# Performance work log

Measured on AMD Instinct MI355X. Metric: run time of the kernel, lower is better.

The kernel has to match this reference:

```python
import jax, jax.numpy as jnp
import numpy as np

B, S, D, H, P, K = 2, 1025, 1024, 16, 1024, 32
HD = D // H
G = int(np.sqrt(P))
TEMP = 0.1
CANTOR_W = 0.3
SCALE = HD ** -0.5
EPS_LN = 1e-5


def _layernorm(x, w, b):
    m = jnp.mean(x, axis=-1, keepdims=True)
    v = jnp.mean((x - m) ** 2, axis=-1, keepdims=True)
    return (x - m) * jax.lax.rsqrt(v + EPS_LN) * w + b


def _l2norm(x):
    n = jnp.sqrt(jnp.sum(x * x, axis=-1, keepdims=True))
    return x / jnp.maximum(n, 1e-12)


def _cantor_bias():
    idx = np.arange(P)
    xg, yg = idx % G, idx // G
    s = xg + yg
    z = (s * (s + 1) // 2 + yg).astype(np.float32)
    fp = z / max(z.max(), 1.0)
    dist = np.abs(fp[None, :] - fp[:, None])
    aff = 1.0 - dist
    np.fill_diagonal(aff, -1e9)
    return jnp.asarray(aff * CANTOR_W, dtype=jnp.float32)


def setup_inputs() -> dict:
    key = jax.random.key(0)
    ks = jax.random.split(key, 16)
    std = 0.02
    def w(k, *shape):
        return jax.random.normal(k, shape, dtype=jnp.float32) * std
    inp = {
        'x': jax.random.normal(ks[0], (B, S, D), dtype=jnp.float32),
        'norm1_w': jnp.ones((D,), jnp.float32), 'norm1_b': jnp.zeros((D,), jnp.float32),
        'rq_w': w(ks[1], D, D), 'rq_b': jnp.zeros((D,), jnp.float32),
        'rk_w': w(ks[2], D, D), 'rk_b': jnp.zeros((D,), jnp.float32),
        'pos_bias': _cantor_bias(),
        'qkv_w': w(ks[3], 3 * D, D), 'qkv_b': jnp.zeros((3 * D,), jnp.float32),
        'proj_w': w(ks[4], D, D), 'proj_b': jnp.zeros((D,), jnp.float32),
        'norm2_w': jnp.ones((D,), jnp.float32), 'norm2_b': jnp.zeros((D,), jnp.float32),
        'fc1_w': w(ks[5], 4 * D, D), 'fc1_b': jnp.zeros((4 * D,), jnp.float32),
        'fc2_w': w(ks[6], D, 4 * D), 'fc2_b': jnp.zeros((D,), jnp.float32),
    }
    return inp


def reference(x, norm1_w, norm1_b, rq_w, rq_b, rk_w, rk_b, pos_bias,
              qkv_w, qkv_b, proj_w, proj_b, norm2_w, norm2_b,
              fc1_w, fc1_b, fc2_w, fc2_b):
    x_norm = _layernorm(x, norm1_w, norm1_b)
    # ---- router: content-based top-k wormhole routes over patches ----
    xp = x_norm[:, 1:, :]                                   # [B,P,D]
    q_r = _l2norm(xp @ rq_w.T + rq_b)
    k_r = _l2norm(xp @ rk_w.T + rk_b)
    scores = jnp.einsum('bpd,bqd->bpq', q_r, k_r) + pos_bias[None]
    eye = jnp.eye(P, dtype=bool)
    scores = jnp.where(eye[None], -1e9, scores)
    topk_scores, routes = jax.lax.top_k(scores / TEMP, K)   # [B,P,K]
    route_w = jax.nn.softmax(topk_scores, axis=-1)          # [B,P,K]
    # ---- qkv ----
    qkv = (x_norm @ qkv_w.T + qkv_b).reshape(B, S, 3, H, HD)
    qkv = jnp.transpose(qkv, (2, 0, 3, 1, 4))               # [3,B,H,S,hd]
    Q, Kf, V = qkv[0], qkv[1], qkv[2]
    # CLS token: dense attention over all positions
    Qc = Q[:, :, :1, :]
    attn_cls = jax.nn.softmax(jnp.einsum('bhqd,bhkd->bhqk', Qc, Kf) * SCALE, axis=-1)
    out_cls = jnp.einsum('bhqk,bhkd->bhqd', attn_cls, V)    # [B,H,1,hd]
    # Patches: sparse gather attention via wormhole routes
    Qp, Kp, Vp = Q[:, :, 1:], Kf[:, :, 1:], V[:, :, 1:]     # [B,H,P,hd]
    gather = jax.vmap(lambda t, r: t[:, r])                 # t:[H,P,hd], r:[P,K] -> [H,P,K,hd]
    Kg = gather(Kp, routes)                                  # [B,H,P,K,hd]
    Vg = gather(Vp, routes)
    sp = jnp.einsum('bhpd,bhpkd->bhpk', Qp, Kg) * SCALE
    sp = sp + jnp.clip(jnp.log(route_w), -10.0, None)[:, None]
    attn_p = jax.nn.softmax(sp, axis=-1)
    out_p = jnp.einsum('bhpk,bhpkd->bhpd', attn_p, Vg)      # [B,H,P,hd]
    out = jnp.concatenate([out_cls, out_p], axis=2)          # [B,H,S,hd]
    out = jnp.transpose(out, (0, 2, 1, 3)).reshape(B, S, D)
    x = x + (out @ proj_w.T + proj_b)
    h = _layernorm(x, norm2_w, norm2_b)
    h = jax.nn.gelu(h @ fc1_w.T + fc1_b, approximate=False)
    x = x + (h @ fc2_w.T + fc2_b)
    return x
```

## Files before the change

### kernel.cpp

```cpp
#include <hip/hip_runtime.h>
#include <hip/hip_bf16.h>
#include <math.h>

typedef unsigned short u16;
typedef __attribute__((ext_vector_type(8))) short short8;
typedef __attribute__((ext_vector_type(4))) float f32x4;

#define B_ 2
#define S_ 1025
#define D_ 1024
#define H_ 16
#define HD_ 64
#define P_ 1024
#define K_ 32
#define NS_ 16

static constexpr float TEMP_ = 0.1f;
static constexpr float SCALE_ = 0.125f;
static constexpr float EPS_LN_ = 1e-5f;

__device__ __forceinline__ float bf2f(u16 u) {
  unsigned int t = ((unsigned int)u) << 16;
  float f;
  __builtin_memcpy(&f, &t, 4);
  return f;
}
__device__ __forceinline__ u16 f2bf(float f) {
  __hip_bfloat16 h = __float2bfloat16(f);
  u16 u;
  __builtin_memcpy(&u, &h, 2);
  return u;
}
__device__ __forceinline__ float gelu_f(float x) {
  return 0.5f * x * (1.0f + erff(x * 0.70710678118654752f));
}

typedef __attribute__((address_space(1))) const unsigned int gas_u32;
typedef __attribute__((address_space(3))) unsigned int las_u32;
__device__ __forceinline__ void g2l16(const void* g, void* l) {
  __builtin_amdgcn_global_load_lds((gas_u32*)g, (las_u32*)l, 16, 0, 0);
}

__global__ __launch_bounds__(256) void conv4_kernel(
    const float* __restrict__ s0, int n0, const float* __restrict__ s1, int n1,
    const float* __restrict__ s2, int n2, const float* __restrict__ s3, int n3,
    u16* __restrict__ dst) {
  const int e = (blockIdx.x * 256 + threadIdx.x) * 4;
  const float* src;
  int off;
  if (e < n0) { src = s0; off = e; }
  else if (e < n0 + n1) { src = s1; off = e - n0; }
  else if (e < n0 + n1 + n2) { src = s2; off = e - n0 - n1; }
  else if (e < n0 + n1 + n2 + n3) { src = s3; off = e - n0 - n1 - n2; }
  else return;
  float4 t = *reinterpret_cast<const float4*>(src + off);
  ushort4 o;
  o.x = f2bf(t.x); o.y = f2bf(t.y); o.z = f2bf(t.z); o.w = f2bf(t.w);
  *reinterpret_cast<ushort4*>(dst + e) = o;
}

__global__ __launch_bounds__(256) void init_addb(const float* __restrict__ a,
                                                 const float* __restrict__ bias,
                                                 float* __restrict__ out) {
  const long long base = (long long)blockIdx.x * D_;
#pragma unroll
  for (int u = 0; u < 4; ++u) {
    int d = threadIdx.x + u * 256;
    out[base + d] = a[base + d] + bias[d];
  }
}

__global__ __launch_bounds__(256) void init_scores(const float* __restrict__ pos,
                                                   float* __restrict__ scores) {
  const int bp = blockIdx.x;
  const int p = bp & (P_ - 1);
  const long long base = (long long)bp * P_;
#pragma unroll
  for (int u = 0; u < 4; ++u) {
    int q = threadIdx.x + u * 256;
    float v = pos[(long long)p * P_ + q];
    if (p == q) v = -1e9f;
    scores[base + q] = v;
  }
}

__device__ __forceinline__ float block_sum256(float v, float* red4) {
  for (int off = 32; off > 0; off >>= 1) v += __shfl_down(v, off);
  if ((threadIdx.x & 63) == 0) red4[threadIdx.x >> 6] = v;
  __syncthreads();
  float r = red4[0] + red4[1] + red4[2] + red4[3];
  __syncthreads();
  return r;
}
__device__ __forceinline__ float block_max256(float v, float* red4) {
  for (int off = 32; off > 0; off >>= 1) v = fmaxf(v, __shfl_down(v, off));
  if ((threadIdx.x & 63) == 0) red4[threadIdx.x >> 6] = v;
  __syncthreads();
  float r = fmaxf(fmaxf(red4[0], red4[1]), fmaxf(red4[2], red4[3]));
  __syncthreads();
  return r;
}

__global__ __launch_bounds__(256) void ln_kernel(const float* __restrict__ x,
                                                 const float* __restrict__ w,
                                                 const float* __restrict__ b,
                                                 u16* __restrict__ out) {
  __shared__ float red4[4];
  const long long base = (long long)blockIdx.x * D_;
  float v[4];
  float s = 0.f, ss = 0.f;
#pragma unroll
  for (int u = 0; u < 4; ++u) {
    int d = threadIdx.x + u * 256;
    float f = x[base + d];
    v[u] = f; s += f; ss += f * f;
  }
  float tot = block_sum256(s, red4);
  float tot2 = block_sum256(ss, red4);
  float mean = tot * (1.0f / D_);
  float var = tot2 * (1.0f / D_) - mean * mean;
  float rstd = rsqrtf(var + EPS_LN_);
#pragma unroll
  for (int u = 0; u < 4; ++u) {
    int d = threadIdx.x + u * 256;
    out[base + d] = f2bf((v[u] - mean) * rstd * w[d] + b[d]);
  }
}

__global__ __launch_bounds__(256) void l2norm2_kernel(u16* __restrict__ qr,
                                                      u16* __restrict__ kr) {
  __shared__ float red4[4];
  const int row = blockIdx.x;
  u16* x = (row < 2048) ? qr + (long long)row * D_
                        : kr + (long long)(row - 2048) * D_;
  float v[4];
  float ss = 0.f;
#pragma unroll
  for (int u = 0; u < 4; ++u) {
    int d = threadIdx.x + u * 256;
    v[u] = bf2f(x[d]);
    ss += v[u] * v[u];
  }
  float tot = block_sum256(ss, red4);
  float inv = 1.0f / fmaxf(sqrtf(tot), 1e-12f);
#pragma unroll
  for (int u = 0; u < 4; ++u) {
    int d = threadIdx.x + u * 256;
    x[d] = f2bf(v[u] * inv);
  }
}

template <int MODE>
__device__ __forceinline__ void gemm_body(
    u16* sA, u16* sW,
    const u16* __restrict__ A, long long a_off, const u16* __restrict__ W,
    int N, int M, int Kd, int klen, int rpb, long long a_bs, long long w_bs,
    const float* __restrict__ bias, const float* __restrict__ bias2, int bias_off,
    u16* __restrict__ outU, u16* __restrict__ outU2, float* __restrict__ outF,
    int bx, int by, int bz) {
  const int tid = threadIdx.x;
  const int lane = tid & 63;
  const int q4 = lane >> 4;
  const int r16 = lane & 15;
  const int wave = tid >> 6;
  const int wr = (wave & 1) * 32;
  const int wc = (wave >> 1) * 64;
  const int row0 = by * 64;
  const int col0 = bx * 128;
  const int batch = row0 / rpb;
  const u16* Ab = A + a_off + (long long)batch * a_bs +
                  (long long)(row0 - batch * rpb) * Kd;
  const u16* Wb = W + (long long)batch * w_bs + (long long)col0 * Kd;
  const int rmax = N - 1 - row0;
  const int srow = tid >> 3;
  const int kx = ((tid & 7) ^ (srow & 7)) * 8;
  const int kbeg = bz * klen;
  const int niter = klen >> 6;
  f32x4 acc[2][4] = {};
  for (int it = 0; it < niter; ++it) {
    const int k0 = kbeg + it * 64;
#pragma unroll
    for (int c = 0; c < 2; ++c) {
      const int rg = c * 32 + srow;
      g2l16(Ab + (long long)min(rg, rmax) * Kd + kx + k0, &sA[c * 2048 + tid * 8]);
    }
#pragma unroll
    for (int c = 0; c < 4; ++c) {
      const int rg = c * 32 + srow;
      g2l16(Wb + (long long)rg * Kd + kx + k0, &sW[c * 2048 + tid * 8]);
    }
    __builtin_amdgcn_s_waitcnt(0);
    __syncthreads();
#pragma unroll
    for (int s = 0; s < 2; ++s) {
      short8 a[2], b[4];
      const int ks = ((s * 4 + q4) ^ (r16 & 7)) * 8;
#pragma unroll
      for (int i = 0; i < 2; ++i)
        a[i] = *reinterpret_cast<const short8*>(&sA[(wr + i * 16 + r16) * 64 + ks]);
#pragma unroll
      for (int j = 0; j < 4; ++j)
        b[j] = *reinterpret_cast<const short8*>(&sW[(wc + j * 16 + r16) * 64 + ks]);
#pragma unroll
      for (int i = 0; i < 2; ++i)
#pragma unroll
        for (int j = 0; j < 4; ++j)
          acc[i][j] = __builtin_amdgcn_mfma_f32_16x16x32_bf16(a[i], b[j],
                                                              acc[i][j], 0, 0, 0);
    }
    __syncthreads();
  }
#pragma unroll
  for (int i = 0; i < 2; ++i) {
#pragma unroll
    for (int reg = 0; reg < 4; ++reg) {
      const int n = row0 + wr + i * 16 + q4 * 4 + reg;
      if (n >= N) continue;
      const long long nrow = (long long)n * M;
#pragma unroll
      for (int j = 0; j < 4; ++j) {
        const int m = col0 + wc + j * 16 + r16;
        float v = acc[i][j][reg];
        if (MODE == 0) {
          if (m < 1024) outU[(long long)n * 1024 + m] = f2bf(v + bias[m]);
          else outU2[(long long)n * 1024 + m - 1024] = f2bf(v + bias2[m - 1024]);
        } else if (MODE == 2) {
          outU[nrow + m] = f2bf(v + bias[bias_off + m]);
        } else if (MODE == 3) {
          outU[nrow + m] = f2bf(gelu_f(v + bias[bias_off + m]));
        } else {
          unsafeAtomicAdd(&outF[nrow + m], v);
        }
      }
    }
  }
}

__device__ __forceinline__ int xcd_swz(int orig, int nwg) {
  return (orig & 7) * (nwg >> 3) + (orig >> 3);
}

template <int MODE>
__global__ __launch_bounds__(256, 6) void mfma_gemm(
    const u16* __restrict__ A, long long a_off, const u16* __restrict__ W,
    int N, int M, int Kd, int klen, int rpb, long long a_bs, long long w_bs,
    const float* __restrict__ bias, const float* __restrict__ bias2, int bias_off,
    u16* __restrict__ outU, u16* __restrict__ outU2, float* __restrict__ outF) {
  __shared__ u16 sA[64 * 64];
  __shared__ u16 sW[128 * 64];
  const int gx = gridDim.x, gy = gridDim.y;
  const int nwg = gx * gy * gridDim.z;
  const int orig = blockIdx.x + gx * (blockIdx.y + gy * blockIdx.z);
  const int swz = xcd_swz(orig, nwg);
  const int bx = swz % gx;
  const int t = swz / gx;
  const int by = t % gy;
  const int bz = t / gy;
  gemm_body<MODE>(sA, sW, A, a_off, W, N, M, Kd, klen, rpb, a_bs, w_bs,
                  bias, bias2, bias_off, outU, outU2, outF, bx, by, bz);
}

__global__ __launch_bounds__(256, 6) void fused_rqk_qkv(
    const u16* __restrict__ xnorm, const u16* __restrict__ wslot,
    const float* __restrict__ rq_b, const float* __restrict__ rk_b,
    const float* __restrict__ qkv_b,
    u16* __restrict__ qr, u16* __restrict__ kr, u16* __restrict__ qkvb) {
  __shared__ u16 sA[64 * 64];
  __shared__ u16 sW[128 * 64];
  const int id = xcd_swz(blockIdx.x, 1304);
  if (id < 512) {
    gemm_body<0>(sA, sW, xnorm, 1024LL, wslot,
                 2048, 2048, 1024, 1024, 1024, (long long)S_ * D_, 0LL,
                 rq_b, rk_b, 0, qr, kr, nullptr, id & 15, id >> 4, 0);
  } else {
    const int id2 = id - 512;
    gemm_body<2>(sA, sW, xnorm, 0LL, wslot + (2 << 20),
                 2050, 3072, 1024, 1024, 2050, 0LL, 0LL,
                 qkv_b, nullptr, 0, qkvb, nullptr, nullptr, id2 % 24, id2 / 24, 0);
  }
}

__global__ __launch_bounds__(256) void topk_kernel(const float* __restrict__ scores,
                                                   int* __restrict__ routes,
                                                   float* __restrict__ logw) {
  const int row = blockIdx.x * 4 + (threadIdx.x >> 6);
  const int lane = threadIdx.x & 63;
  const float* sr = scores + (long long)row * P_;
  float v[16];
#pragma unroll
  for (int j = 0; j < 16; ++j) v[j] = sr[j * 64 + lane];
  float selv = 0.f;
  int seli = 0;
  for (int t = 0; t < K_; ++t) {
    float bv = v[0];
    int bj = 0;
#pragma unroll
    for (int j = 1; j < 16; ++j)
      if (v[j] > bv) { bv = v[j]; bj = j; }
    int bi = bj * 64 + lane;
#pragma unroll
    for (int off = 1; off < 64; off <<= 1) {
      float ov = __shfl_xor(bv, off);
      int oi = __shfl_xor(bi, off);
      if (ov > bv || (ov == bv && oi < bi)) { bv = ov; bi = oi; }
    }
    if (lane == t) { selv = bv; seli = bi; }
    if ((bi & 63) == lane) v[bi >> 6] = -3.0e38f;
  }
  const float sc = selv * (1.0f / TEMP_);
  const float mt = __shfl(sc, 0);
  float e = (lane < K_) ? expf(sc - mt) : 0.f;
  float sum = e;
#pragma unroll
  for (int off = 1; off < 64; off <<= 1) sum += __shfl_xor(sum, off);
  if (lane < K_) {
    const float lw = sc - mt - logf(sum);
    logw[(long long)row * K_ + lane] = fmaxf(lw, -10.0f);
    routes[(long long)row * K_ + lane] = seli;
  }
}

__global__ __launch_bounds__(256) void attn_cls_p1(const u16* __restrict__ qkv,
                                                   float* __restrict__ part) {
  __shared__ float qs[HD_];
  __shared__ float lg[65];
  __shared__ float red4[4];
  __shared__ float sacc[4][HD_];
  const int ck = blockIdx.x;
  const int bh = blockIdx.y;
  const int b = bh >> 4, h = bh & 15;
  const int tid = threadIdx.x;
  const int lane = tid & 63;
  const int wv = tid >> 6;
  const int s0 = ck * 65;
  const int rows = min(65, S_ - s0);
  const long long base = (long long)b * S_ * 3072;
  if (tid < HD_) qs[tid] = bf2f(qkv[base + h * HD_ + tid]);
  __syncthreads();
  float lmax = -3.0e38f;
  if (tid < rows) {
    const u16* kp = qkv + base + (long long)(s0 + tid) * 3072 + 1024 + h * HD_;
    float d = 0.f;
#pragma unroll
    for (int c = 0; c < 8; ++c) {
      short8 kv = *reinterpret_cast<const short8*>(kp + c * 8);
#pragma unroll
      for (int e = 0; e < 8; ++e) d += qs[c * 8 + e] * bf2f((u16)kv[e]);
    }
    d *= SCALE_;
    lg[tid] = d;
    lmax = d;
  }
  const float m = block_max256(lmax, red4);
  float e = 0.f;
  if (tid < rows) {
    e = expf(lg[tid] - m);
    lg[tid] = e;
  }
  const float l = block_sum256(e, red4);
  __syncthreads();
  float acc = 0.f;
  for (int r = wv; r < rows; r += 4)
    acc += lg[r] * bf2f(qkv[base + (long long)(s0 + r) * 3072 + 2048 + h * HD_ + lane]);
  sacc[wv][lane] = acc;
  __syncthreads();
  float* pc = part + ((long long)bh * NS_ + ck) * 66;
  if (tid < HD_)
    pc[tid] = sacc[0][tid] + sacc[1][tid] + sacc[2][tid] + sacc[3][tid];
  if (tid == 64) pc[64] = m;
  if (tid == 65) pc[65] = l;
}

__global__ __launch_bounds__(64) void attn_cls_p2(const float* __restrict__ part,
                                                  u16* __restrict__ out) {
  const int bh = blockIdx.x;
  const int b = bh >> 4, h = bh & 15;
  const int tid = threadIdx.x;
  const float* pb = part + (long long)bh * NS_ * 66;
  float M = -3.0e38f;
#pragma unroll
  for (int c = 0; c < NS_; ++c) M = fmaxf(M, pb[c * 66 + 64]);
  float L = 0.f, a = 0.f;
#pragma unroll
  for (int c = 0; c < NS_; ++c) {
    const float w = expf(pb[c * 66 + 64] - M);
    L += pb[c * 66 + 65] * w;
    a += pb[c * 66 + tid] * w;
  }
  out[(long long)b * S_ * D_ + h * HD_ + tid] = f2bf(a / L);
}

__global__ __launch_bounds__(64) void attn_patch_kernel(const u16* __restrict__ qkv,
                                                        const int* __restrict__ routes,
                                                        const float* __restrict__ logw,
                                                        u16* __restrict__ out) {
  __shared__ float qs[HD_];
  __shared__ float wk[K_];
  __shared__ int sidx[K_];
  const int bid = blockIdx.x;
  const int h = bid & 15;
  const int p = (bid >> 4) & (P_ - 1);
  const int b = bid >> 14;
  const int tid = threadIdx.x;
  const long long base = (long long)b * S_ * 3072;
  qs[tid] = bf2f(qkv[base + (long long)(1 + p) * 3072 + h * HD_ + tid]);
  __syncthreads();
  float lg = -3.0e38f;
  if (tid < K_) {
    const long long ro = ((long long)(b * P_ + p)) * K_ + tid;
    const int r = routes[ro];
    sidx[tid] = r;
    const u16* kp = qkv + base + (long long)(1 + r) * 3072 + 1024 + h * HD_;
    float d = 0.f;
#pragma unroll
    for (int c = 0; c < 8; ++c) {
      short8 kv = *reinterpret_cast<const short8*>(kp + c * 8);
#pragma unroll
      for (int e = 0; e < 8; ++e) d += qs[c * 8 + e] * bf2f((u16)kv[e]);
    }
    lg = d * SCALE_ + logw[ro];
  }
  float m = lg;
#pragma unroll
  for (int off = 1; off < 32; off <<= 1) m = fmaxf(m, __shfl_xor(m, off));
  float e = (tid < K_) ? expf(lg - m) : 0.f;
  float sum = e;
#pragma unroll
  for (int off = 1; off < 32; off <<= 1) sum += __shfl_xor(sum, off);
  if (tid < K_) wk[tid] = e / sum;
  __syncthreads();
  float acc = 0.f;
#pragma unroll 4
  for (int k = 0; k < K_; ++k)
    acc += wk[k] * bf2f(qkv[base + (long long)(1 + sidx[k]) * 3072 + 2048 + h * HD_ + tid]);
  out[((long long)b * S_ + 1 + p) * D_ + h * HD_ + tid] = f2bf(acc);
}

extern "C" void kernel_launch(void* const* d_in, const int* in_sizes, int n_in,
                              void* d_out, int out_size, void* d_ws, size_t ws_size,
                              hipStream_t stream) {
  const float* x      = (const float*)d_in[0];
  const float* n1w    = (const float*)d_in[1];
  const float* n1b    = (const float*)d_in[2];
  const float* rq_w   = (const float*)d_in[3];
  const float* rq_b   = (const float*)d_in[4];
  const float* rk_w   = (const float*)d_in[5];
  const float* rk_b   = (const float*)d_in[6];
  const float* pos    = (const float*)d_in[7];
  const float* qkv_w  = (const float*)d_in[8];
  const float* qkv_b  = (const float*)d_in[9];
  const float* proj_w = (const float*)d_in[10];
  const float* proj_b = (const float*)d_in[11];
  const float* n2w    = (const float*)d_in[12];
  const float* n2b    = (const float*)d_in[13];
  const float* fc1_w  = (const float*)d_in[14];
  const float* fc1_b  = (const float*)d_in[15];
  const float* fc2_w  = (const float*)d_in[16];
  const float* fc2_b  = (const float*)d_in[17];
  float* out = (float*)d_out;

  char* mem = (char*)d_ws;
  int*   routes = (int*)mem;
  float* logw   = (float*)(mem + 262144);
  float* part   = (float*)(mem + 524288);
  u16*   wslot  = (u16*)(mem + 786432);
  u16*   xnorm  = (u16*)(mem + 17563648);
  u16*   qr     = (u16*)(mem + 21762048);
  u16*   attn   = qr;
  u16*   qkvb   = (u16*)(mem + 25960448);
  u16*   kr     = (u16*)(mem + 38555648);
  u16*   hbuf   = qkvb;
  float* scores = (float*)(mem + 42758144);
  float* x1     = (float*)(mem + 42758144);

  ln_kernel<<<B_ * S_, 256, 0, stream>>>(x, n1w, n1b, xnorm);

  conv4_kernel<<<6144, 256, 0, stream>>>(rq_w, 1 << 20, rk_w, 1 << 20,
                                         qkv_w, 3 << 20, proj_w, 1 << 20, wslot);

  fused_rqk_qkv<<<1304, 256, 0, stream>>>(xnorm, wslot, rq_b, rk_b, qkv_b,
                                          qr, kr, qkvb);

  l2norm2_kernel<<<4096, 256, 0, stream>>>(qr, kr);

  init_scores<<<B_ * P_, 256, 0, stream>>>(pos, scores);
  mfma_gemm<5><<<dim3(8, 32, 2), 256, 0, stream>>>(qr, 0LL, kr,
      2048, 1024, 1024, 512, 1024, 1LL << 20, 1LL << 20,
      nullptr, nullptr, 0, nullptr, nullptr, scores);

  topk_kernel<<<512, 256, 0, stream>>>(scores, routes, logw);

  attn_cls_p1<<<dim3(NS_, B_ * H_), 256, 0, stream>>>(qkvb, part);
  attn_cls_p2<<<B_ * H_, 64, 0, stream>>>(part, attn);
  attn_patch_kernel<<<B_ * P_ * H_, 64, 0, stream>>>(qkvb, routes, logw, attn);

  init_addb<<<B_ * S_, 256, 0, stream>>>(x, proj_b, x1);
  mfma_gemm<5><<<dim3(8, 33, 2), 256, 0, stream>>>(attn, 0LL, wslot + (5 << 20),
      2050, 1024, 1024, 512, 2050, 0LL, 0LL,
      nullptr, nullptr, 0, nullptr, nullptr, x1);

  conv4_kernel<<<8192, 256, 0, stream>>>(fc1_w, 1 << 22, fc2_w, 1 << 22,
                                         nullptr, 0, nullptr, 0, wslot);

  ln_kernel<<<B_ * S_, 256, 0, stream>>>(x1, n2w, n2b, xnorm);

  mfma_gemm<3><<<dim3(32, 33), 256, 0, stream>>>(xnorm, 0LL, wslot,
      2050, 4096, 1024, 1024, 2050, 0LL, 0LL,
      fc1_b, nullptr, 0, hbuf, nullptr, nullptr);
  init_addb<<<B_ * S_, 256, 0, stream>>>(x1, fc2_b, out);
  mfma_gemm<5><<<dim3(8, 33, 4), 256, 0, stream>>>(hbuf, 0LL, wslot + (1 << 22),
      2050, 1024, 4096, 1024, 2050, 0LL, 0LL,
      nullptr, nullptr, 0, nullptr, nullptr, out);
}
```

Before: 404.1 us.

## Replace split-K atomics with partial buffers reduced in consumer kernels

```diff
diff --git a/kernel.cpp b/kernel.cpp
--- a/kernel.cpp
+++ b/kernel.cpp
@@ -59,31 +59,6 @@
   *reinterpret_cast<ushort4*>(dst + e) = o;
 }
 
-__global__ __launch_bounds__(256) void init_addb(const float* __restrict__ a,
-                                                 const float* __restrict__ bias,
-                                                 float* __restrict__ out) {
-  const long long base = (long long)blockIdx.x * D_;
-#pragma unroll
-  for (int u = 0; u < 4; ++u) {
-    int d = threadIdx.x + u * 256;
-    out[base + d] = a[base + d] + bias[d];
-  }
-}
-
-__global__ __launch_bounds__(256) void init_scores(const float* __restrict__ pos,
-                                                   float* __restrict__ scores) {
-  const int bp = blockIdx.x;
-  const int p = bp & (P_ - 1);
-  const long long base = (long long)bp * P_;
-#pragma unroll
-  for (int u = 0; u < 4; ++u) {
-    int q = threadIdx.x + u * 256;
-    float v = pos[(long long)p * P_ + q];
-    if (p == q) v = -1e9f;
-    scores[base + q] = v;
-  }
-}
-
 __device__ __forceinline__ float block_sum256(float v, float* red4) {
   for (int off = 32; off > 0; off >>= 1) v += __shfl_down(v, off);
   if ((threadIdx.x & 63) == 0) red4[threadIdx.x >> 6] = v;
@@ -124,6 +99,46 @@
   for (int u = 0; u < 4; ++u) {
     int d = threadIdx.x + u * 256;
     out[base + d] = f2bf((v[u] - mean) * rstd * w[d] + b[d]);
+  }
+}
+
+__global__ __launch_bounds__(256) void ln2res_kernel(
+    const float* __restrict__ x, const float* __restrict__ pb,
+    const float* __restrict__ p0, const float* __restrict__ p1,
+    const float* __restrict__ w, const float* __restrict__ b,
+    float* __restrict__ x1, u16* __restrict__ out) {
+  __shared__ float red4[4];
+  const long long base = (long long)blockIdx.x * D_;
+  float v[4];
+  float s = 0.f, ss = 0.f;
+#pragma unroll
+  for (int u = 0; u < 4; ++u) {
+    int d = threadIdx.x + u * 256;
+    float f = x[base + d] + pb[d] + p0[base + d] + p1[base + d];
+    x1[base + d] = f;
+    v[u] = f; s += f; ss += f * f;
+  }
+  float tot = block_sum256(s, red4);
+  float tot2 = block_sum256(ss, red4);
+  float mean = tot * (1.0f / D_);
+  float var = tot2 * (1.0f / D_) - mean * mean;
+  float rstd = rsqrtf(var + EPS_LN_);
+#pragma unroll
+  for (int u = 0; u < 4; ++u) {
+    int d = threadIdx.x + u * 256;
+    out[base + d] = f2bf((v[u] - mean) * rstd * w[d] + b[d]);
+  }
+}
+
+__global__ __launch_bounds__(256) void fc2red_kernel(
+    const float* __restrict__ x1, const float* __restrict__ b,
+    const float* __restrict__ p0, const float* __restrict__ p1,
+    float* __restrict__ out) {
+  const long long base = (long long)blockIdx.x * D_;
+#pragma unroll
+  for (int u = 0; u < 4; ++u) {
+    int d = threadIdx.x + u * 256;
+    out[base + d] = x1[base + d] + b[d] + p0[base + d] + p1[base + d];
   }
 }
 
@@ -210,6 +225,7 @@
     }
     __syncthreads();
   }
+  const long long sbase = (MODE == 6) ? (long long)bz * bias_off : 0;
 #pragma unroll
   for (int i = 0; i < 2; ++i) {
 #pragma unroll
@@ -229,7 +245,7 @@
         } else if (MODE == 3) {
           outU[nrow + m] = f2bf(gelu_f(v + bias[bias_off + m]));
         } else {
-          unsafeAtomicAdd(&outF[nrow + m], v);
+          outF[sbase + nrow + m] = v;
         }
       }
     }
@@ -280,15 +296,24 @@
   }
 }
 
-__global__ __launch_bounds__(256) void topk_kernel(const float* __restrict__ scores,
+__global__ __launch_bounds__(256) void topk_kernel(const float* __restrict__ s0,
+                                                   const float* __restrict__ s1,
+                                                   const float* __restrict__ pos,
                                                    int* __restrict__ routes,
                                                    float* __restrict__ logw) {
   const int row = blockIdx.x * 4 + (threadIdx.x >> 6);
   const int lane = threadIdx.x & 63;
-  const float* sr = scores + (long long)row * P_;
+  const int p = row & (P_ - 1);
+  const float* r0 = s0 + (long long)row * P_;
+  const float* r1 = s1 + (long long)row * P_;
+  const float* pr = pos + (long long)p * P_;
   float v[16];
 #pragma unroll
-  for (int j = 0; j < 16; ++j) v[j] = sr[j * 64 + lane];
+  for (int j = 0; j < 16; ++j) {
+    const int q = j * 64 + lane;
+    float t = r0[q] + r1[q] + pr[q];
+    v[j] = (q == p) ? -1e9f : t;
+  }
   float selv = 0.f;
   int seli = 0;
   for (int t = 0; t < K_; ++t) {
@@ -470,8 +495,13 @@
   u16*   qkvb   = (u16*)(mem + 25960448);
   u16*   kr     = (u16*)(mem + 38555648);
   u16*   hbuf   = qkvb;
-  float* scores = (float*)(mem + 42758144);
   float* x1     = (float*)(mem + 42758144);
+  float* sc_p0 = (float*)(mem + 786432);
+  float* sc_p1 = (float*)(mem + 42758144);
+  float* pr_p0 = (float*)(mem + 25960448);
+  float* pr_p1 = (float*)(mem + 34357248);
+  float* fc_p0 = (float*)(mem + 0);
+  float* fc_p1 = (float*)(mem + 17563648);
 
   ln_kernel<<<B_ * S_, 256, 0, stream>>>(x, n1w, n1b, xnorm);
 
@@ -483,32 +513,31 @@
 
   l2norm2_kernel<<<4096, 256, 0, stream>>>(qr, kr);
 
-  init_scores<<<B_ * P_, 256, 0, stream>>>(pos, scores);
-  mfma_gemm<5><<<dim3(8, 32, 2), 256, 0, stream>>>(qr, 0LL, kr,
+  mfma_gemm<6><<<dim3(8, 32, 2), 256, 0, stream>>>(qr, 0LL, kr,
       2048, 1024, 1024, 512, 1024, 1LL << 20, 1LL << 20,
-      nullptr, nullptr, 0, nullptr, nullptr, scores);
-
-  topk_kernel<<<512, 256, 0, stream>>>(scores, routes, logw);
+      nullptr, nullptr, 10492928, nullptr, nullptr, sc_p0);
+
+  topk_kernel<<<512, 256, 0, stream>>>(sc_p0, sc_p1, pos, routes, logw);
 
   attn_cls_p1<<<dim3(NS_, B_ * H_), 256, 0, stream>>>(qkvb, part);
   attn_cls_p2<<<B_ * H_, 64, 0, stream>>>(part, attn);
   attn_patch_kernel<<<B_ * P_ * H_, 64, 0, stream>>>(qkvb, routes, logw, attn);
 
-  init_addb<<<B_ * S_, 256, 0, stream>>>(x, proj_b, x1);
-  mfma_gemm<5><<<dim3(8, 33, 2), 256, 0, stream>>>(attn, 0LL, wslot + (5 << 20),
+  mfma_gemm<6><<<dim3(8, 33, 2), 256, 0, stream>>>(attn, 0LL, wslot + (5 << 20),
       2050, 1024, 1024, 512, 2050, 0LL, 0LL,
-      nullptr, nullptr, 0, nullptr, nullptr, x1);
+      nullptr, nullptr, 2099200, nullptr, nullptr, pr_p0);
 
   conv4_kernel<<<8192, 256, 0, stream>>>(fc1_w, 1 << 22, fc2_w, 1 << 22,
                                          nullptr, 0, nullptr, 0, wslot);
 
-  ln_kernel<<<B_ * S_, 256, 0, stream>>>(x1, n2w, n2b, xnorm);
+  ln2res_kernel<<<B_ * S_, 256, 0, stream>>>(x, proj_b, pr_p0, pr_p1,
+                                             n2w, n2b, x1, xnorm);
 
   mfma_gemm<3><<<dim3(32, 33), 256, 0, stream>>>(xnorm, 0LL, wslot,
       2050, 4096, 1024, 1024, 2050, 0LL, 0LL,
       fc1_b, nullptr, 0, hbuf, nullptr, nullptr);
-  init_addb<<<B_ * S_, 256, 0, stream>>>(x1, fc2_b, out);
-  mfma_gemm<5><<<dim3(8, 33, 4), 256, 0, stream>>>(hbuf, 0LL, wslot + (1 << 22),
-      2050, 1024, 4096, 1024, 2050, 0LL, 0LL,
-      nullptr, nullptr, 0, nullptr, nullptr, out);
-}
+  mfma_gemm<6><<<dim3(8, 33, 2), 256, 0, stream>>>(hbuf, 0LL, wslot + (1 << 22),
+      2050, 1024, 4096, 2048, 2050, 0LL, 0LL,
+      nullptr, nullptr, 4390912, nullptr, nullptr, fc_p0);
+  fc2red_kernel<<<B_ * S_, 256, 0, stream>>>(x1, fc2_b, fc_p0, fc_p1, out);
+}
```

New measurement: 380.0 us, median of 2. 1.06x faster.
